# Kernel tuning notes

Measured on AMD Instinct MI355X. Metric: run time of the kernel, lower is better.

## Reference

```python
import jax, jax.numpy as jnp
import numpy as np

EPS = 1e-12  # F.normalize eps


def sage_conv(x, src, dst, n_nodes, W_l, b_l, W_r):
    """PyG SAGEConv with mean aggregation and L2 normalize.
    out = lin_l(mean_{j in N(i)} x_j) + lin_r(x_i), then row-wise L2 normalize.
    """
    # mean-aggregate neighbor features: scatter-add then divide by in-degree
    msg_sum = jax.ops.segment_sum(x[src], dst, num_segments=n_nodes)  # [N, F]
    deg = jax.ops.segment_sum(jnp.ones_like(dst, dtype=x.dtype), dst,
                              num_segments=n_nodes)                   # [N]
    agg = msg_sum / jnp.maximum(deg, 1.0)[:, None]
    out = agg @ W_l + b_l + x @ W_r                                   # [N, out]
    norm = jnp.sqrt(jnp.sum(out * out, axis=-1, keepdims=True))
    return out / jnp.maximum(norm, EPS)


def setup_inputs() -> dict:
    key = jax.random.key(0)
    ks = jax.random.split(key, 8)
    N, E, D_IN, D_H, D_OUT = 100000, 320000, 256, 64, 4
    x = jax.random.normal(ks[0], (N, D_IN), dtype=jnp.float32)
    edge_index = jax.random.randint(ks[1], (2, E), 0, N, dtype=jnp.int32)
    s1 = 1.0 / np.sqrt(D_IN)
    s2 = 1.0 / np.sqrt(D_H)
    W1_l = jax.random.uniform(ks[2], (D_IN, D_H), jnp.float32, -s1, s1)
    b1_l = jnp.zeros((D_H,), jnp.float32)
    W1_r = jax.random.uniform(ks[3], (D_IN, D_H), jnp.float32, -s1, s1)
    W2_l = jax.random.uniform(ks[4], (D_H, D_OUT), jnp.float32, -s2, s2)
    b2_l = jnp.zeros((D_OUT,), jnp.float32)
    W2_r = jax.random.uniform(ks[5], (D_H, D_OUT), jnp.float32, -s2, s2)
    return {"x": x, "edge_index": edge_index,
            "W1_l": W1_l, "b1_l": b1_l, "W1_r": W1_r,
            "W2_l": W2_l, "b2_l": b2_l, "W2_r": W2_r}


def reference(x, edge_index, W1_l, b1_l, W1_r, W2_l, b2_l, W2_r):
    # eval mode: dropout is identity
    n_nodes = x.shape[0]
    src, dst = edge_index[0], edge_index[1]
    h = jax.nn.relu(sage_conv(x, src, dst, n_nodes, W1_l, b1_l, W1_r))
    out = sage_conv(h, src, dst, n_nodes, W2_l, b2_l, W2_r)
    return out
```

## Files before the change

kernel.cpp:

```cpp
#include <hip/hip_runtime.h>

#define DIN 256
#define DH  64
#define DOUT 4

typedef __attribute__((ext_vector_type(8))) short bf16x8;
typedef __attribute__((ext_vector_type(4))) float f32x4;

__device__ __forceinline__ short f2bf(float f) {
    unsigned int u = __float_as_uint(f);
    unsigned int r = (u + 0x7FFFu + ((u >> 16) & 1u)) >> 16;
    return (short)r;
}
__device__ __forceinline__ float bf2f(short h) {
    return __uint_as_float(((unsigned int)(unsigned short)h) << 16);
}

__global__ void count_kernel(const int* __restrict__ dst, int* __restrict__ cnt, int E) {
    int e = blockIdx.x * blockDim.x + threadIdx.x;
    if (e < E) atomicAdd(&cnt[dst[e]], 1);
}

__global__ void scan_a_kernel(const int* __restrict__ cnt, int* __restrict__ blocksum, int N) {
    __shared__ int s[256];
    const int t = threadIdx.x;
    const int gi = blockIdx.x * 256 + t;
    s[t] = (gi < N) ? cnt[gi] : 0;
    __syncthreads();
    for (int stp = 128; stp > 0; stp >>= 1) {
        if (t < stp) s[t] += s[t + stp];
        __syncthreads();
    }
    if (t == 0) blocksum[blockIdx.x] = s[0];
}

__global__ void scan_b_kernel(int* __restrict__ blocksum, int* __restrict__ blockoff, int nblk) {
    __shared__ int s[1024];
    const int t = threadIdx.x;
    int v = (t < nblk) ? blocksum[t] : 0;
    s[t] = v;
    __syncthreads();
    for (int stp = 1; stp < 1024; stp <<= 1) {
        int add = (t >= stp) ? s[t - stp] : 0;
        __syncthreads();
        s[t] += add;
        __syncthreads();
    }
    if (t < nblk) blockoff[t] = s[t] - v;
}

__global__ void scan_c_kernel(const int* __restrict__ cnt, const int* __restrict__ blockoff,
                              int* __restrict__ off, int N) {
    __shared__ int s[256];
    const int t = threadIdx.x;
    const int gi = blockIdx.x * 256 + t;
    int v = (gi < N) ? cnt[gi] : 0;
    s[t] = v;
    __syncthreads();
    for (int stp = 1; stp < 256; stp <<= 1) {
        int add = (t >= stp) ? s[t - stp] : 0;
        __syncthreads();
        s[t] += add;
        __syncthreads();
    }
    if (gi <= N) off[gi] = blockoff[blockIdx.x] + s[t] - v;
}

__global__ void fill_kernel(const int* __restrict__ src, const int* __restrict__ dst,
                            const int* __restrict__ off, int* __restrict__ cursor,
                            int* __restrict__ nbr, int E) {
    int e = blockIdx.x * blockDim.x + threadIdx.x;
    if (e >= E) return;
    const int d = dst[e];
    const int p = atomicAdd(&cursor[d], 1);
    nbr[off[d] + p] = src[e];
}

__global__ void wprep_kernel(const float* __restrict__ Wl, const float* __restrict__ Wr,
                             short* __restrict__ WTh, short* __restrict__ WTl) {
    const int k = threadIdx.x;
    const int n = blockIdx.x;
    const float v = (n < 64) ? Wl[k * 64 + n] : Wr[k * 64 + (n - 64)];
    const short hi = f2bf(v);
    const short lo = f2bf(v - bf2f(hi));
    WTh[n * 256 + k] = hi;
    WTl[n * 256 + k] = lo;
}

#define XS_LD 40
__global__ __launch_bounds__(256) void gemm1_mfma(
    const float* __restrict__ x, const short* __restrict__ WTh,
    const short* __restrict__ WTl, float* __restrict__ y, int N)
{
    __shared__ short xsh[64 * XS_LD];
    __shared__ short xsl[64 * XS_LD];
    __shared__ short wth[128 * XS_LD];
    __shared__ short wtl[128 * XS_LD];

    const int tid  = threadIdx.x;
    const int wave = tid >> 6;
    const int lane = tid & 63;
    const int lm   = lane & 15;
    const int quad = lane >> 4;
    const int brow = blockIdx.x * 64;

    f32x4 acc[4][2];
    #pragma unroll
    for (int mt = 0; mt < 4; ++mt)
        #pragma unroll
        for (int nt = 0; nt < 2; ++nt)
            acc[mt][nt] = (f32x4){0.f, 0.f, 0.f, 0.f};

    const int xr  = tid >> 2;
    const int xkp = (tid & 3) * 8;
    const int wn  = tid >> 1;
    const int wkp = (tid & 1) * 16;

    for (int kc = 0; kc < DIN; kc += 32) {
        {
            const int row_g = brow + xr;
            float4 f0, f1;
            if (row_g < N) {
                const float4* xp = (const float4*)(x + (size_t)row_g * DIN + kc + xkp);
                f0 = xp[0]; f1 = xp[1];
            } else {
                f0 = f1 = make_float4(0.f, 0.f, 0.f, 0.f);
            }
            bf16x8 ph, pl;
            float fv[8] = {f0.x, f0.y, f0.z, f0.w, f1.x, f1.y, f1.z, f1.w};
            #pragma unroll
            for (int j = 0; j < 8; ++j) {
                const short hi = f2bf(fv[j]);
                ph[j] = hi;
                pl[j] = f2bf(fv[j] - bf2f(hi));
            }
            *(bf16x8*)(&xsh[xr * XS_LD + xkp]) = ph;
            *(bf16x8*)(&xsl[xr * XS_LD + xkp]) = pl;
        }
        {
            const size_t gw = (size_t)wn * 256 + kc + wkp;
            const bf16x8* wph = (const bf16x8*)(WTh + gw);
            const bf16x8* wpl = (const bf16x8*)(WTl + gw);
            *(bf16x8*)(&wth[wn * XS_LD + wkp])     = wph[0];
            *(bf16x8*)(&wth[wn * XS_LD + wkp + 8]) = wph[1];
            *(bf16x8*)(&wtl[wn * XS_LD + wkp])     = wpl[0];
            *(bf16x8*)(&wtl[wn * XS_LD + wkp + 8]) = wpl[1];
        }
        __syncthreads();

        bf16x8 ah[4], al[4], bh[2], bl[2];
        #pragma unroll
        for (int mt = 0; mt < 4; ++mt) {
            const int off2 = (mt * 16 + lm) * XS_LD + quad * 8;
            ah[mt] = *(const bf16x8*)(&xsh[off2]);
            al[mt] = *(const bf16x8*)(&xsl[off2]);
        }
        #pragma unroll
        for (int nt = 0; nt < 2; ++nt) {
            const int off2 = (wave * 32 + nt * 16 + lm) * XS_LD + quad * 8;
            bh[nt] = *(const bf16x8*)(&wth[off2]);
            bl[nt] = *(const bf16x8*)(&wtl[off2]);
        }
        #pragma unroll
        for (int mt = 0; mt < 4; ++mt)
            #pragma unroll
            for (int nt = 0; nt < 2; ++nt) {
                acc[mt][nt] = __builtin_amdgcn_mfma_f32_16x16x32_bf16(
                    ah[mt], bh[nt], acc[mt][nt], 0, 0, 0);
                acc[mt][nt] = __builtin_amdgcn_mfma_f32_16x16x32_bf16(
                    ah[mt], bl[nt], acc[mt][nt], 0, 0, 0);
                acc[mt][nt] = __builtin_amdgcn_mfma_f32_16x16x32_bf16(
                    al[mt], bh[nt], acc[mt][nt], 0, 0, 0);
            }
        __syncthreads();
    }

    #pragma unroll
    for (int mt = 0; mt < 4; ++mt) {
        #pragma unroll
        for (int r = 0; r < 4; ++r) {
            const int row_g = brow + mt * 16 + quad * 4 + r;
            if (row_g < N) {
                const int col = wave * 32 + lm;
                float* yp = y + (size_t)row_g * 128 + col;
                yp[0]  = acc[mt][0][r];
                yp[16] = acc[mt][1][r];
            }
        }
    }
}

__global__ __launch_bounds__(256) void fused1_kernel(
    const float* __restrict__ y, const int* __restrict__ off, const int* __restrict__ nbr,
    const float* __restrict__ b1, const float* __restrict__ W2l, const float* __restrict__ W2r,
    float* __restrict__ z, int N)
{
    const int wave = threadIdx.x >> 6;
    const int lane = threadIdx.x & 63;
    const int i = blockIdx.x * 4 + wave;
    if (i >= N) return;

    const int beg = off[i];
    const int end = off[i + 1];
    const int deg = end - beg;

    const int dd = (deg < 64) ? deg : 64;
    int myn = (lane < dd) ? nbr[beg + lane] : 0;

    float acc = 0.f;
    int j = 0;
    for (; j + 1 < dd; j += 2) {
        const int s0 = __shfl(myn, j, 64);
        const int s1 = __shfl(myn, j + 1, 64);
        const float v0 = y[(size_t)s0 * 128 + lane];
        const float v1 = y[(size_t)s1 * 128 + lane];
        acc += v0 + v1;
    }
    if (j < dd) {
        const int s0 = __shfl(myn, j, 64);
        acc += y[(size_t)s0 * 128 + lane];
    }
    for (int q = beg + 64; q < end; ++q) {
        const int s = nbr[q];
        acc += y[(size_t)s * 128 + lane];
    }

    const float dinv = 1.0f / fmaxf((float)deg, 1.0f);
    float v = acc * dinv + b1[lane] + y[(size_t)i * 128 + 64 + lane];

    float ss = v * v;
    #pragma unroll
    for (int m = 32; m >= 1; m >>= 1) ss += __shfl_xor(ss, m, 64);
    const float inv = 1.0f / fmaxf(sqrtf(ss), 1e-12f);
    const float hv = fmaxf(v * inv, 0.f);

    const float4 wl = *(const float4*)(W2l + lane * 4);
    const float4 wr = *(const float4*)(W2r + lane * 4);
    float p0 = hv * wl.x, p1 = hv * wl.y, p2 = hv * wl.z, p3 = hv * wl.w;
    float p4 = hv * wr.x, p5 = hv * wr.y, p6 = hv * wr.z, p7 = hv * wr.w;

    const bool b0 = (lane & 1) != 0;
    float s0_ = b0 ? p0 : p4;
    float s1_ = b0 ? p1 : p5;
    float s2_ = b0 ? p2 : p6;
    float s3_ = b0 ? p3 : p7;
    float q0 = (b0 ? p4 : p0) + __shfl_xor(s0_, 1, 64);
    float q1 = (b0 ? p5 : p1) + __shfl_xor(s1_, 1, 64);
    float q2 = (b0 ? p6 : p2) + __shfl_xor(s2_, 1, 64);
    float q3 = (b0 ? p7 : p3) + __shfl_xor(s3_, 1, 64);
    const bool b1b = (lane & 2) != 0;
    float t0 = b1b ? q0 : q2;
    float t1 = b1b ? q1 : q3;
    float r0 = (b1b ? q2 : q0) + __shfl_xor(t0, 2, 64);
    float r1 = (b1b ? q3 : q1) + __shfl_xor(t1, 2, 64);
    const bool b2 = (lane & 4) != 0;
    float u0 = b2 ? r0 : r1;
    float zv = (b2 ? r1 : r0) + __shfl_xor(u0, 4, 64);
    zv += __shfl_xor(zv, 8, 64);
    zv += __shfl_xor(zv, 16, 64);
    zv += __shfl_xor(zv, 32, 64);
    const int ch = 4 * (lane & 1) + ((lane & 2)) + ((lane >> 2) & 1);
    if (lane < 8) z[(size_t)i * 8 + ch] = zv;
}

__global__ void fused2_kernel(const float* __restrict__ z, const int* __restrict__ off,
                              const int* __restrict__ nbr, const float* __restrict__ b2,
                              float* __restrict__ out, int N)
{
    const int i = blockIdx.x * blockDim.x + threadIdx.x;
    if (i >= N) return;
    const int beg = off[i];
    const int end = off[i + 1];
    float4 acc = make_float4(0.f, 0.f, 0.f, 0.f);
    for (int j = beg; j < end; ++j) {
        const int s = nbr[j];
        const float4 t = *(const float4*)(z + (size_t)s * 8);
        acc.x += t.x; acc.y += t.y; acc.z += t.z; acc.w += t.w;
    }
    const float dinv = 1.0f / fmaxf((float)(end - beg), 1.0f);
    const float4 r  = *(const float4*)(z + (size_t)i * 8 + 4);
    const float4 bb = *(const float4*)(b2);
    float4 o;
    o.x = acc.x * dinv + bb.x + r.x;
    o.y = acc.y * dinv + bb.y + r.y;
    o.z = acc.z * dinv + bb.z + r.z;
    o.w = acc.w * dinv + bb.w + r.w;
    const float ss = o.x * o.x + o.y * o.y + o.z * o.z + o.w * o.w;
    const float inv = 1.0f / fmaxf(sqrtf(ss), 1e-12f);
    o.x *= inv; o.y *= inv; o.z *= inv; o.w *= inv;
    *(float4*)(out + (size_t)i * 4) = o;
}

extern "C" void kernel_launch(void* const* d_in, const int* in_sizes, int n_in,
                              void* d_out, int out_size, void* d_ws, size_t ws_size,
                              hipStream_t stream)
{
    const float* x    = (const float*)d_in[0];
    const int*   ei   = (const int*)d_in[1];
    const float* W1l  = (const float*)d_in[2];
    const float* b1l  = (const float*)d_in[3];
    const float* W1r  = (const float*)d_in[4];
    const float* W2l  = (const float*)d_in[5];
    const float* b2l  = (const float*)d_in[6];
    const float* W2r  = (const float*)d_in[7];
    float* out = (float*)d_out;

    const int N = in_sizes[0] / DIN;
    const int E = in_sizes[1] / 2;
    const int* src = ei;
    const int* dst = ei + E;
    const int nblk = (N + 255) / 256;

    char* ws = (char*)d_ws;
    size_t woff = 0;
    auto alloc = [&](size_t bytes) {
        void* p = ws + woff;
        woff += (bytes + 255) & ~(size_t)255;
        return p;
    };
    float* y        = (float*)alloc((size_t)N * 128 * 4);
    float* z        = (float*)alloc((size_t)N * 8 * 4);
    short* WTh      = (short*)alloc((size_t)128 * 256 * 2);
    short* WTl      = (short*)alloc((size_t)128 * 256 * 2);
    int*   cnt      = (int*)alloc((size_t)N * 4);
    int*   cursor   = (int*)alloc((size_t)N * 4);
    int*   off      = (int*)alloc((size_t)(N + 1) * 4);
    int*   nbr      = (int*)alloc((size_t)E * 4);
    int*   blocksum = (int*)alloc((size_t)nblk * 4);
    int*   blockoff = (int*)alloc((size_t)nblk * 4);

    hipMemsetAsync(cnt,    0, (size_t)N * 4, stream);
    hipMemsetAsync(cursor, 0, (size_t)N * 4, stream);

    count_kernel<<<(E + 255) / 256, 256, 0, stream>>>(dst, cnt, E);
    scan_a_kernel<<<nblk, 256, 0, stream>>>(cnt, blocksum, N);
    scan_b_kernel<<<1, 1024, 0, stream>>>(blocksum, blockoff, nblk);
    scan_c_kernel<<<nblk, 256, 0, stream>>>(cnt, blockoff, off, N);
    fill_kernel<<<(E + 255) / 256, 256, 0, stream>>>(src, dst, off, cursor, nbr, E);

    wprep_kernel<<<128, 256, 0, stream>>>(W1l, W1r, WTh, WTl);
    gemm1_mfma<<<(N + 63) / 64, 256, 0, stream>>>(x, WTh, WTl, y, N);

    fused1_kernel<<<(N + 3) / 4, 256, 0, stream>>>(y, off, nbr, b1l, W2l, W2r, z, N);

    fused2_kernel<<<(N + 255) / 256, 256, 0, stream>>>(z, off, nbr, b2l, out, N);
}
```

Measured before the change: 275.6 us.

## Double-buffer x tiles in gemm1, load W fragments directly to registers

Restructures the first GEMM so the next K-chunk of x and W is prefetched into registers while MFMAs run on the current chunk, with x staged in a double-buffered LDS tile. W operands skip LDS and come straight from global memory into registers. The kernel drops one barrier per iteration, switches the bf16 split to truncation, and adds an occupancy hint. It also merges the two memsets into one. Truncation slightly changes the hi/lo split rounding, though hi+lo still carries most of the fp32 precision.

```diff
diff --git a/kernel.cpp b/kernel.cpp
--- a/kernel.cpp
+++ b/kernel.cpp
@@ -11,6 +11,9 @@
     unsigned int u = __float_as_uint(f);
     unsigned int r = (u + 0x7FFFu + ((u >> 16) & 1u)) >> 16;
     return (short)r;
+}
+__device__ __forceinline__ short f2bf_trunc(float f) {
+    return (short)(__float_as_uint(f) >> 16);
 }
 __device__ __forceinline__ float bf2f(short h) {
     return __uint_as_float(((unsigned int)(unsigned short)h) << 16);
@@ -88,14 +91,12 @@
 }
 
 #define XS_LD 40
-__global__ __launch_bounds__(256) void gemm1_mfma(
+__global__ __launch_bounds__(256, 4) void gemm1_mfma(
     const float* __restrict__ x, const short* __restrict__ WTh,
     const short* __restrict__ WTl, float* __restrict__ y, int N)
 {
-    __shared__ short xsh[64 * XS_LD];
-    __shared__ short xsl[64 * XS_LD];
-    __shared__ short wth[128 * XS_LD];
-    __shared__ short wtl[128 * XS_LD];
+    __shared__ short xsh[2][64 * XS_LD];
+    __shared__ short xsl[2][64 * XS_LD];
 
     const int tid  = threadIdx.x;
     const int wave = tid >> 6;
@@ -104,6 +105,17 @@
     const int quad = lane >> 4;
     const int brow = blockIdx.x * 64;
 
+    const int xr    = tid >> 2;
+    const int xk    = (tid & 3) * 8;
+    const int row_g = brow + xr;
+    const bool xvalid = (row_g < N);
+    const float* xptr = x + (size_t)row_g * DIN + xk;
+    const int xs_off = xr * XS_LD + xk;
+
+    const int col0 = wave * 32 + lm;
+    const size_t wb0 = (size_t)col0 * 256 + quad * 8;
+    const size_t wb1 = (size_t)(col0 + 16) * 256 + quad * 8;
+
     f32x4 acc[4][2];
     #pragma unroll
     for (int mt = 0; mt < 4; ++mt)
@@ -111,78 +123,96 @@
         for (int nt = 0; nt < 2; ++nt)
             acc[mt][nt] = (f32x4){0.f, 0.f, 0.f, 0.f};
 
-    const int xr  = tid >> 2;
-    const int xkp = (tid & 3) * 8;
-    const int wn  = tid >> 1;
-    const int wkp = (tid & 1) * 16;
-
-    for (int kc = 0; kc < DIN; kc += 32) {
-        {
-            const int row_g = brow + xr;
-            float4 f0, f1;
-            if (row_g < N) {
-                const float4* xp = (const float4*)(x + (size_t)row_g * DIN + kc + xkp);
-                f0 = xp[0]; f1 = xp[1];
+    {
+        float4 a, b;
+        if (xvalid) {
+            a = ((const float4*)xptr)[0];
+            b = ((const float4*)xptr)[1];
+        } else {
+            a = b = make_float4(0.f, 0.f, 0.f, 0.f);
+        }
+        bf16x8 ph, pl;
+        float fv[8] = {a.x, a.y, a.z, a.w, b.x, b.y, b.z, b.w};
+        #pragma unroll
+        for (int j = 0; j < 8; ++j) {
+            const short hi = f2bf_trunc(fv[j]);
+            ph[j] = hi;
+            pl[j] = f2bf_trunc(fv[j] - bf2f(hi));
+        }
+        *(bf16x8*)(&xsh[0][xs_off]) = ph;
+        *(bf16x8*)(&xsl[0][xs_off]) = pl;
+    }
+    bf16x8 wh_cur[2], wl_cur[2];
+    wh_cur[0] = *(const bf16x8*)(WTh + wb0);
+    wh_cur[1] = *(const bf16x8*)(WTh + wb1);
+    wl_cur[0] = *(const bf16x8*)(WTl + wb0);
+    wl_cur[1] = *(const bf16x8*)(WTl + wb1);
+    __syncthreads();
+
+    #pragma unroll
+    for (int k = 0; k < 8; ++k) {
+        const int buf = k & 1;
+
+        float4 na, nb;
+        bf16x8 wh_nxt[2], wl_nxt[2];
+        if (k < 7) {
+            const int kc = (k + 1) * 32;
+            if (xvalid) {
+                na = ((const float4*)(xptr + kc))[0];
+                nb = ((const float4*)(xptr + kc))[1];
             } else {
-                f0 = f1 = make_float4(0.f, 0.f, 0.f, 0.f);
-            }
-            bf16x8 ph, pl;
-            float fv[8] = {f0.x, f0.y, f0.z, f0.w, f1.x, f1.y, f1.z, f1.w};
-            #pragma unroll
-            for (int j = 0; j < 8; ++j) {
-                const short hi = f2bf(fv[j]);
-                ph[j] = hi;
-                pl[j] = f2bf(fv[j] - bf2f(hi));
-            }
-            *(bf16x8*)(&xsh[xr * XS_LD + xkp]) = ph;
-            *(bf16x8*)(&xsl[xr * XS_LD + xkp]) = pl;
-        }
-        {
-            const size_t gw = (size_t)wn * 256 + kc + wkp;
-            const bf16x8* wph = (const bf16x8*)(WTh + gw);
-            const bf16x8* wpl = (const bf16x8*)(WTl + gw);
-            *(bf16x8*)(&wth[wn * XS_LD + wkp])     = wph[0];
-            *(bf16x8*)(&wth[wn * XS_LD + wkp + 8]) = wph[1];
-            *(bf16x8*)(&wtl[wn * XS_LD + wkp])     = wpl[0];
-            *(bf16x8*)(&wtl[wn * XS_LD + wkp + 8]) = wpl[1];
-        }
-        __syncthreads();
-
-        bf16x8 ah[4], al[4], bh[2], bl[2];
+                na = nb = make_float4(0.f, 0.f, 0.f, 0.f);
+            }
+            wh_nxt[0] = *(const bf16x8*)(WTh + wb0 + kc);
+            wh_nxt[1] = *(const bf16x8*)(WTh + wb1 + kc);
+            wl_nxt[0] = *(const bf16x8*)(WTl + wb0 + kc);
+            wl_nxt[1] = *(const bf16x8*)(WTl + wb1 + kc);
+        }
+
         #pragma unroll
         for (int mt = 0; mt < 4; ++mt) {
-            const int off2 = (mt * 16 + lm) * XS_LD + quad * 8;
-            ah[mt] = *(const bf16x8*)(&xsh[off2]);
-            al[mt] = *(const bf16x8*)(&xsl[off2]);
-        }
-        #pragma unroll
-        for (int nt = 0; nt < 2; ++nt) {
-            const int off2 = (wave * 32 + nt * 16 + lm) * XS_LD + quad * 8;
-            bh[nt] = *(const bf16x8*)(&wth[off2]);
-            bl[nt] = *(const bf16x8*)(&wtl[off2]);
-        }
-        #pragma unroll
-        for (int mt = 0; mt < 4; ++mt)
+            const int aoff = (mt * 16 + lm) * XS_LD + quad * 8;
+            const bf16x8 ah = *(const bf16x8*)(&xsh[buf][aoff]);
+            const bf16x8 al = *(const bf16x8*)(&xsl[buf][aoff]);
             #pragma unroll
             for (int nt = 0; nt < 2; ++nt) {
                 acc[mt][nt] = __builtin_amdgcn_mfma_f32_16x16x32_bf16(
-                    ah[mt], bh[nt], acc[mt][nt], 0, 0, 0);
+                    ah, wh_cur[nt], acc[mt][nt], 0, 0, 0);
                 acc[mt][nt] = __builtin_amdgcn_mfma_f32_16x16x32_bf16(
-                    ah[mt], bl[nt], acc[mt][nt], 0, 0, 0);
+                    ah, wl_cur[nt], acc[mt][nt], 0, 0, 0);
                 acc[mt][nt] = __builtin_amdgcn_mfma_f32_16x16x32_bf16(
-                    al[mt], bh[nt], acc[mt][nt], 0, 0, 0);
-            }
-        __syncthreads();
+                    al, wh_cur[nt], acc[mt][nt], 0, 0, 0);
+            }
+        }
+
+        if (k < 7) {
+            bf16x8 ph, pl;
+            float fv[8] = {na.x, na.y, na.z, na.w, nb.x, nb.y, nb.z, nb.w};
+            #pragma unroll
+            for (int j = 0; j < 8; ++j) {
+                const short hi = f2bf_trunc(fv[j]);
+                ph[j] = hi;
+                pl[j] = f2bf_trunc(fv[j] - bf2f(hi));
+            }
+            *(bf16x8*)(&xsh[buf ^ 1][xs_off]) = ph;
+            *(bf16x8*)(&xsl[buf ^ 1][xs_off]) = pl;
+            #pragma unroll
+            for (int nt = 0; nt < 2; ++nt) {
+                wh_cur[nt] = wh_nxt[nt];
+                wl_cur[nt] = wl_nxt[nt];
+            }
+            __syncthreads();
+        }
     }
 
     #pragma unroll
     for (int mt = 0; mt < 4; ++mt) {
         #pragma unroll
         for (int r = 0; r < 4; ++r) {
-            const int row_g = brow + mt * 16 + quad * 4 + r;
-            if (row_g < N) {
+            const int rg = brow + mt * 16 + quad * 4 + r;
+            if (rg < N) {
                 const int col = wave * 32 + lm;
-                float* yp = y + (size_t)row_g * 128 + col;
+                float* yp = y + (size_t)rg * 128 + col;
                 yp[0]  = acc[mt][0][r];
                 yp[16] = acc[mt][1][r];
             }
@@ -322,15 +352,14 @@
     float* z        = (float*)alloc((size_t)N * 8 * 4);
     short* WTh      = (short*)alloc((size_t)128 * 256 * 2);
     short* WTl      = (short*)alloc((size_t)128 * 256 * 2);
-    int*   cnt      = (int*)alloc((size_t)N * 4);
-    int*   cursor   = (int*)alloc((size_t)N * 4);
+    int*   cnt      = (int*)alloc((size_t)2 * N * 4);
+    int*   cursor   = cnt + N;
     int*   off      = (int*)alloc((size_t)(N + 1) * 4);
     int*   nbr      = (int*)alloc((size_t)E * 4);
     int*   blocksum = (int*)alloc((size_t)nblk * 4);
     int*   blockoff = (int*)alloc((size_t)nblk * 4);
 
-    hipMemsetAsync(cnt,    0, (size_t)N * 4, stream);
-    hipMemsetAsync(cursor, 0, (size_t)N * 4, stream);
+    hipMemsetAsync(cnt, 0, (size_t)2 * N * 4, stream);
 
     count_kernel<<<(E + 255) / 256, 256, 0, stream>>>(dst, cnt, E);
     scan_a_kernel<<<nblk, 256, 0, stream>>>(cnt, blocksum, N);
```

After: 273.5 us. About the same (-0.7%).

## Drop LDS staging in gemm1, load operands directly into registers with prefetch

Applied to the files above, without the earlier changes.

The layer-1 GEMM no longer stages x and the split-bf16 weights through shared memory. Each wave now loads its 32 rows of x straight into MFMA fragment registers with a one-step prefetch, and reads the 128 weight columns from global/L2 with a rolling prefetch. This removes the barriers and LDS round trips. Rounding in the hi/lo split becomes truncation, and the two memsets are merged into one. The cost is more registers (launch bounds set to 3 blocks), repeated weight loads per wave, and slightly different split precision.

```diff
diff --git a/kernel.cpp b/kernel.cpp
--- a/kernel.cpp
+++ b/kernel.cpp
@@ -11,6 +11,9 @@
     unsigned int u = __float_as_uint(f);
     unsigned int r = (u + 0x7FFFu + ((u >> 16) & 1u)) >> 16;
     return (short)r;
+}
+__device__ __forceinline__ short f2bf_trunc(float f) {
+    return (short)(__float_as_uint(f) >> 16);
 }
 __device__ __forceinline__ float bf2f(short h) {
     return __uint_as_float(((unsigned int)(unsigned short)h) << 16);
@@ -87,104 +90,93 @@
     WTl[n * 256 + k] = lo;
 }
 
-#define XS_LD 40
-__global__ __launch_bounds__(256) void gemm1_mfma(
+__global__ __launch_bounds__(256, 3) void gemm1_mfma(
     const float* __restrict__ x, const short* __restrict__ WTh,
     const short* __restrict__ WTl, float* __restrict__ y, int N)
 {
-    __shared__ short xsh[64 * XS_LD];
-    __shared__ short xsl[64 * XS_LD];
-    __shared__ short wth[128 * XS_LD];
-    __shared__ short wtl[128 * XS_LD];
-
     const int tid  = threadIdx.x;
     const int wave = tid >> 6;
     const int lane = tid & 63;
     const int lm   = lane & 15;
     const int quad = lane >> 4;
-    const int brow = blockIdx.x * 64;
-
-    f32x4 acc[4][2];
+    const int wrow = blockIdx.x * 128 + wave * 32;
+
+    const int r0 = wrow + lm;
+    const int r1 = wrow + 16 + lm;
+    const float* xp0 = x + (size_t)((r0 < N) ? r0 : (N - 1)) * DIN + quad * 8;
+    const float* xp1 = x + (size_t)((r1 < N) ? r1 : (N - 1)) * DIN + quad * 8;
+
+    f32x4 acc[2][8];
     #pragma unroll
-    for (int mt = 0; mt < 4; ++mt)
+    for (int mt = 0; mt < 2; ++mt)
         #pragma unroll
-        for (int nt = 0; nt < 2; ++nt)
+        for (int nt = 0; nt < 8; ++nt)
             acc[mt][nt] = (f32x4){0.f, 0.f, 0.f, 0.f};
 
-    const int xr  = tid >> 2;
-    const int xkp = (tid & 3) * 8;
-    const int wn  = tid >> 1;
-    const int wkp = (tid & 1) * 16;
-
-    for (int kc = 0; kc < DIN; kc += 32) {
+    float4 a0a = ((const float4*)xp0)[0];
+    float4 a0b = ((const float4*)xp0)[1];
+    float4 a1a = ((const float4*)xp1)[0];
+    float4 a1b = ((const float4*)xp1)[1];
+
+    #pragma unroll
+    for (int k = 0; k < 8; ++k) {
+        float4 n0a, n0b, n1a, n1b;
+        if (k < 7) {
+            const int kc = (k + 1) * 32;
+            n0a = ((const float4*)(xp0 + kc))[0];
+            n0b = ((const float4*)(xp0 + kc))[1];
+            n1a = ((const float4*)(xp1 + kc))[0];
+            n1b = ((const float4*)(xp1 + kc))[1];
+        }
+
+        bf16x8 ah0, al0, ah1, al1;
         {
-            const int row_g = brow + xr;
-            float4 f0, f1;
-            if (row_g < N) {
-                const float4* xp = (const float4*)(x + (size_t)row_g * DIN + kc + xkp);
-                f0 = xp[0]; f1 = xp[1];
-            } else {
-                f0 = f1 = make_float4(0.f, 0.f, 0.f, 0.f);
-            }
-            bf16x8 ph, pl;
-            float fv[8] = {f0.x, f0.y, f0.z, f0.w, f1.x, f1.y, f1.z, f1.w};
+            float f0[8] = {a0a.x, a0a.y, a0a.z, a0a.w, a0b.x, a0b.y, a0b.z, a0b.w};
+            float f1[8] = {a1a.x, a1a.y, a1a.z, a1a.w, a1b.x, a1b.y, a1b.z, a1b.w};
             #pragma unroll
             for (int j = 0; j < 8; ++j) {
-                const short hi = f2bf(fv[j]);
-                ph[j] = hi;
-                pl[j] = f2bf(fv[j] - bf2f(hi));
+                short h0 = f2bf_trunc(f0[j]);
+                ah0[j] = h0;
+                al0[j] = f2bf_trunc(f0[j] - bf2f(h0));
+                short h1 = f2bf_trunc(f1[j]);
+                ah1[j] = h1;
+                al1[j] = f2bf_trunc(f1[j] - bf2f(h1));
             }
-            *(bf16x8*)(&xsh[xr * XS_LD + xkp]) = ph;
-            *(bf16x8*)(&xsl[xr * XS_LD + xkp]) = pl;
         }
-        {
-            const size_t gw = (size_t)wn * 256 + kc + wkp;
-            const bf16x8* wph = (const bf16x8*)(WTh + gw);
-            const bf16x8* wpl = (const bf16x8*)(WTl + gw);
-            *(bf16x8*)(&wth[wn * XS_LD + wkp])     = wph[0];
-            *(bf16x8*)(&wth[wn * XS_LD + wkp + 8]) = wph[1];
-            *(bf16x8*)(&wtl[wn * XS_LD + wkp])     = wpl[0];
-            *(bf16x8*)(&wtl[wn * XS_LD + wkp + 8]) = wpl[1];
+
+        const int kc = k * 32 + quad * 8;
+        bf16x8 bh = *(const bf16x8*)(WTh + (size_t)lm * 256 + kc);
+        bf16x8 bl = *(const bf16x8*)(WTl + (size_t)lm * 256 + kc);
+        #pragma unroll
+        for (int nt = 0; nt < 8; ++nt) {
+            bf16x8 bh_n, bl_n;
+            if (nt < 7) {
+                const size_t wb = (size_t)((nt + 1) * 16 + lm) * 256 + kc;
+                bh_n = *(const bf16x8*)(WTh + wb);
+                bl_n = *(const bf16x8*)(WTl + wb);
+            }
+            acc[0][nt] = __builtin_amdgcn_mfma_f32_16x16x32_bf16(ah0, bh, acc[0][nt], 0, 0, 0);
+            acc[0][nt] = __builtin_amdgcn_mfma_f32_16x16x32_bf16(ah0, bl, acc[0][nt], 0, 0, 0);
+            acc[0][nt] = __builtin_amdgcn_mfma_f32_16x16x32_bf16(al0, bh, acc[0][nt], 0, 0, 0);
+            acc[1][nt] = __builtin_amdgcn_mfma_f32_16x16x32_bf16(ah1, bh, acc[1][nt], 0, 0, 0);
+            acc[1][nt] = __builtin_amdgcn_mfma_f32_16x16x32_bf16(ah1, bl, acc[1][nt], 0, 0, 0);
+            acc[1][nt] = __builtin_amdgcn_mfma_f32_16x16x32_bf16(al1, bh, acc[1][nt], 0, 0, 0);
+            bh = bh_n; bl = bl_n;
         }
-        __syncthreads();
-
-        bf16x8 ah[4], al[4], bh[2], bl[2];
-        #pragma unroll
-        for (int mt = 0; mt < 4; ++mt) {
-            const int off2 = (mt * 16 + lm) * XS_LD + quad * 8;
-            ah[mt] = *(const bf16x8*)(&xsh[off2]);
-            al[mt] = *(const bf16x8*)(&xsl[off2]);
-        }
-        #pragma unroll
-        for (int nt = 0; nt < 2; ++nt) {
-            const int off2 = (wave * 32 + nt * 16 + lm) * XS_LD + quad * 8;
-            bh[nt] = *(const bf16x8*)(&wth[off2]);
-            bl[nt] = *(const bf16x8*)(&wtl[off2]);
-        }
-        #pragma unroll
-        for (int mt = 0; mt < 4; ++mt)
-            #pragma unroll
-            for (int nt = 0; nt < 2; ++nt) {
-                acc[mt][nt] = __builtin_amdgcn_mfma_f32_16x16x32_bf16(
-                    ah[mt], bh[nt], acc[mt][nt], 0, 0, 0);
-                acc[mt][nt] = __builtin_amdgcn_mfma_f32_16x16x32_bf16(
-                    ah[mt], bl[nt], acc[mt][nt], 0, 0, 0);
-                acc[mt][nt] = __builtin_amdgcn_mfma_f32_16x16x32_bf16(
-                    al[mt], bh[nt], acc[mt][nt], 0, 0, 0);
-            }
-        __syncthreads();
+
+        if (k < 7) { a0a = n0a; a0b = n0b; a1a = n1a; a1b = n1b; }
     }
 
     #pragma unroll
-    for (int mt = 0; mt < 4; ++mt) {
+    for (int mt = 0; mt < 2; ++mt) {
         #pragma unroll
         for (int r = 0; r < 4; ++r) {
-            const int row_g = brow + mt * 16 + quad * 4 + r;
-            if (row_g < N) {
-                const int col = wave * 32 + lm;
-                float* yp = y + (size_t)row_g * 128 + col;
-                yp[0]  = acc[mt][0][r];
-                yp[16] = acc[mt][1][r];
+            const int rg = wrow + mt * 16 + quad * 4 + r;
+            if (rg < N) {
+                float* yp = y + (size_t)rg * 128 + lm;
+                #pragma unroll
+                for (int nt = 0; nt < 8; ++nt)
+                    yp[nt * 16] = acc[mt][nt][r];
             }
         }
     }
@@ -322,15 +314,14 @@
     float* z        = (float*)alloc((size_t)N * 8 * 4);
     short* WTh      = (short*)alloc((size_t)128 * 256 * 2);
     short* WTl      = (short*)alloc((size_t)128 * 256 * 2);
-    int*   cnt      = (int*)alloc((size_t)N * 4);
-    int*   cursor   = (int*)alloc((size_t)N * 4);
+    int*   cnt      = (int*)alloc((size_t)2 * N * 4);
+    int*   cursor   = cnt + N;
     int*   off      = (int*)alloc((size_t)(N + 1) * 4);
     int*   nbr      = (int*)alloc((size_t)E * 4);
     int*   blocksum = (int*)alloc((size_t)nblk * 4);
     int*   blockoff = (int*)alloc((size_t)nblk * 4);
 
-    hipMemsetAsync(cnt,    0, (size_t)N * 4, stream);
-    hipMemsetAsync(cursor, 0, (size_t)N * 4, stream);
+    hipMemsetAsync(cnt, 0, (size_t)2 * N * 4, stream);
 
     count_kernel<<<(E + 255) / 256, 256, 0, stream>>>(dst, cnt, E);
     scan_a_kernel<<<nblk, 256, 0, stream>>>(cnt, blocksum, N);
@@ -339,7 +330,7 @@
     fill_kernel<<<(E + 255) / 256, 256, 0, stream>>>(src, dst, off, cursor, nbr, E);
 
     wprep_kernel<<<128, 256, 0, stream>>>(W1l, W1r, WTh, WTl);
-    gemm1_mfma<<<(N + 63) / 64, 256, 0, stream>>>(x, WTh, WTl, y, N);
+    gemm1_mfma<<<(N + 127) / 128, 256, 0, stream>>>(x, WTh, WTl, y, N);
 
     fused1_kernel<<<(N + 3) / 4, 256, 0, stream>>>(y, off, nbr, b1l, W2l, W2r, z, N);
 
```

Result: slower. 317.1 us (+15.0%).
